# Performance work log

Measured on AMD Instinct MI355X. Metric: run time of the kernel, lower is better.

## Reference

```python
import jax, jax.numpy as jnp
import numpy as np

B, S, H = 2, 2048, 2048
NH, NKV, HD = 16, 8, 128        # head_dim = H // NH
WINDOW = 1024                    # sliding window size
THETA = 100000.0                 # rope_theta (RotaryEmbedding base)


def setup_inputs() -> dict:
    key = jax.random.key(0)
    ks = jax.random.split(key, 5)
    hidden = jax.random.normal(ks[0], (B, S, H), jnp.float32)
    # fused QKV projection: [H, NH*HD + 2*NKV*HD]
    W_pack = jax.random.normal(ks[1], (H, NH * HD + 2 * NKV * HD), jnp.float32) * (H ** -0.5)
    W_o = jax.random.normal(ks[2], (NH * HD, H), jnp.float32) * ((NH * HD) ** -0.5)
    # per-KV-head 2-tap causal conv weights, softmax-normalized (as in nn.Parameter init)
    conv_k = jax.nn.softmax(jax.random.normal(ks[3], (NKV, 2), jnp.float32), axis=-1)
    conv_v = jax.nn.softmax(jax.random.normal(ks[4], (NKV, 2), jnp.float32), axis=-1)
    return {"hidden": hidden, "W_pack": W_pack, "W_o": W_o, "conv_k": conv_k, "conv_v": conv_v}


def _rope(x, cos, sin):
    # x: (b, s, h, d); cos/sin: (s, d//2); non-interleaved (rotate-half) form
    d2 = x.shape[-1] // 2
    x1, x2 = x[..., :d2], x[..., d2:]
    c = cos[None, :, None, :]
    s = sin[None, :, None, :]
    return jnp.concatenate([x1 * c - x2 * s, x2 * c + x1 * s], axis=-1)


def _causal_conv2(x, w):
    # x: (b, s, kv, d); w: (kv, 2). out[t] = w0*x[t-1] + w1*x[t], zero-padded at t=0
    x_prev = jnp.pad(x, ((0, 0), (1, 0), (0, 0), (0, 0)))[:, :-1]
    return w[None, None, :, 0:1] * x_prev + w[None, None, :, 1:2] * x


def reference(hidden, W_pack, W_o, conv_k, conv_v):
    b, s, _ = hidden.shape
    qkv = hidden @ W_pack                                  # (b, s, NH*HD + 2*NKV*HD)
    q = qkv[..., : NH * HD].reshape(b, s, NH, HD)
    k = qkv[..., NH * HD : NH * HD + NKV * HD].reshape(b, s, NKV, HD)
    v = qkv[..., NH * HD + NKV * HD :].reshape(b, s, NKV, HD)

    inv_freq = 1.0 / (THETA ** (jnp.arange(0, HD, 2, dtype=jnp.float32) / HD))
    freqs = jnp.outer(jnp.arange(s, dtype=jnp.float32), inv_freq)  # (s, HD/2)
    cos, sin = jnp.cos(freqs), jnp.sin(freqs)
    q = _rope(q, cos, sin)
    k = _rope(k, cos, sin)

    # learned 2-tap causal conv mixing adjacent K/V states, per KV head
    k = _causal_conv2(k, conv_k)
    v = _causal_conv2(v, conv_v)

    # GQA: repeat kv heads to match query heads
    group = NH // NKV
    k = jnp.repeat(k, group, axis=2)  # (b, s, NH, HD)
    v = jnp.repeat(v, group, axis=2)

    scores = jnp.einsum('bqhd,bkhd->bhqk', q, k) / jnp.sqrt(jnp.float32(HD))
    i = jnp.arange(s)[:, None]
    j = jnp.arange(s)[None, :]
    mask = (j <= i) & (i - j < WINDOW)  # causal sliding-window mask
    scores = jnp.where(mask[None, None], scores, jnp.finfo(scores.dtype).min)
    probs = jax.nn.softmax(scores, axis=-1)
    out = jnp.einsum('bhqk,bkhd->bqhd', probs, v).reshape(b, s, NH * HD)
    return out @ W_o
```

## Files before the change

kernel.cpp:

```cpp
#include <hip/hip_runtime.h>

#define DI __device__ __forceinline__

typedef unsigned short u16;
typedef __attribute__((ext_vector_type(8))) short s16x8;
typedef __attribute__((ext_vector_type(8))) unsigned short u16x8;
typedef __attribute__((ext_vector_type(4))) float f32x4;
typedef __attribute__((ext_vector_type(16))) float f32x16;

DI u16 f2bf(float x) {
  union { float f; unsigned u; } a; a.f = x;
  unsigned r = a.u + 0x7FFFu + ((a.u >> 16) & 1u);
  return (u16)(r >> 16);
}
DI float bf2f(u16 u) {
  union { unsigned u; float f; } a; a.u = ((unsigned)u) << 16;
  return a.f;
}
DI void gload16(const void* g, void* l) {
  __builtin_amdgcn_global_load_lds(
      (const __attribute__((address_space(1))) unsigned int*)g,
      (__attribute__((address_space(3))) unsigned int*)l, 16, 0, 0);
}
DI f32x4 mfma16(s16x8 a, s16x8 b, f32x4 c) {
  return __builtin_amdgcn_mfma_f32_16x16x32_bf16(a, b, c, 0, 0, 0);
}
DI f32x16 mfma32(s16x8 a, s16x8 b, f32x16 c) {
  return __builtin_amdgcn_mfma_f32_32x32x16_bf16(a, b, c, 0, 0, 0);
}

DI void store4(u16* p, f32x4 v) {
  union { u16 u[4]; unsigned long long ll; } o;
  o.u[0] = f2bf(v[0]); o.u[1] = f2bf(v[1]); o.u[2] = f2bf(v[2]); o.u[3] = f2bf(v[3]);
  *(unsigned long long*)p = o.ll;
}
DI void store4(float* p, f32x4 v) { *(f32x4*)p = v; }

#define SBAR() asm volatile("s_barrier" ::: "memory")

__global__ __launch_bounds__(256) void prep_kernel(
    const float* __restrict__ hidden, const float* __restrict__ W_pack,
    const float* __restrict__ W_o, u16* __restrict__ hA, u16* __restrict__ wpT,
    u16* __restrict__ woT, float* __restrict__ cosT, float* __restrict__ sinT) {
  int bi = blockIdx.x;
  int t = threadIdx.x;
  if (bi < 4096) {
    int i = bi * 256 + t;
    const float4* p = (const float4*)hidden + (size_t)i * 2;
    float4 a = p[0], b = p[1];
    u16x8 o;
    o[0] = f2bf(a.x); o[1] = f2bf(a.y); o[2] = f2bf(a.z); o[3] = f2bf(a.w);
    o[4] = f2bf(b.x); o[5] = f2bf(b.y); o[6] = f2bf(b.z); o[7] = f2bf(b.w);
    *((u16x8*)hA + i) = o;
  } else if (bi < 7168) {
    const float* W; u16* Wt; int R, C, c0, r0;
    if (bi < 6144) {
      int idx = bi - 4096;
      W = W_pack; Wt = wpT; R = 2048; C = 4096;
      c0 = (idx & 63) * 64; r0 = (idx >> 6) * 64;
    } else {
      int idx = bi - 6144;
      W = W_o; Wt = woT; R = 2048; C = 2048;
      c0 = (idx & 31) * 64; r0 = (idx >> 5) * 64;
    }
    __shared__ u16 tile[64][65];
#pragma unroll
    for (int i = 0; i < 16; ++i) {
      int flat = i * 256 + t;
      int r = flat >> 6, c = flat & 63;
      tile[r][c] = f2bf(W[(size_t)(r0 + r) * C + (c0 + c)]);
    }
    __syncthreads();
#pragma unroll
    for (int i = 0; i < 16; ++i) {
      int flat = i * 256 + t;
      int c = flat >> 6, r = flat & 63;
      Wt[(size_t)(c0 + c) * R + (r0 + r)] = tile[r][c];
    }
  } else {
    int i = (bi - 7168) * 256 + t;
    int s = i >> 6, d = i & 63;
    float inv = expf(-(float)d * (11.5129254649702295f / 64.f));
    float f = (float)s * inv;
    cosT[i] = cosf(f);
    sinT[i] = sinf(f);
  }
}

template <typename OutT>
__global__ __launch_bounds__(512, 2) void gemm8p_kernel(
    const u16* __restrict__ A, const u16* __restrict__ Bt, OutT* __restrict__ C,
    int M, int N, int K) {
  __shared__ __align__(16) char lds[131072];
  int nwg = gridDim.x;
  int bid = blockIdx.x;
  int cpx = nwg >> 3;
  int swz = (bid & 7) * cpx + (bid >> 3);
  int ntn = N >> 8;
  int bm = swz / ntn, bn = swz - bm * ntn;
  int m0 = bm << 8, n0 = bn << 8;
  int t = threadIdx.x, w = t >> 6, l = t & 63;
  int wm = w >> 2, wn = w & 3;
  int NT = K >> 6;

  unsigned offA[2][2], offB[2][2];
  int cA[2][2], cB[2][2];
#pragma unroll
  for (int h = 0; h < 2; ++h)
#pragma unroll
    for (int i = 0; i < 2; ++i) {
      int c = i * 16 + h * 8 + w;
      cA[h][i] = c;
      int d = c * 1024 + l * 16;
      int s = d ^ ((((d >> 7) & 7)) << 4);
      offA[h][i] = (unsigned)(m0 + (s >> 7)) * (unsigned)(K * 2) + (unsigned)(s & 127);
      int c2 = ((w >> 2) << 3) + (w & 3) + h * 4 + i * 16;
      cB[h][i] = c2;
      int d2 = c2 * 1024 + l * 16;
      int s2 = d2 ^ ((((d2 >> 7) & 7)) << 4);
      offB[h][i] = (unsigned)(n0 + (s2 >> 7)) * (unsigned)(K * 2) + (unsigned)(s2 & 127);
    }
  const char* Ab = (const char*)A;
  const char* Bb = (const char*)Bt;

#define STAGE_A(tile, h) do { int _t = (tile); if (_t < NT) {                  \
    unsigned _k = (unsigned)_t * 128u;                                          \
    char* _ba = lds + ((_t & 1) << 16);                                         \
    gload16(Ab + (size_t)(offA[h][0] + _k), _ba + cA[h][0] * 1024);             \
    gload16(Ab + (size_t)(offA[h][1] + _k), _ba + cA[h][1] * 1024); } } while (0)
#define STAGE_B(tile, h) do { int _t = (tile); if (_t < NT) {                  \
    unsigned _k = (unsigned)_t * 128u;                                          \
    char* _bb = lds + ((_t & 1) << 16) + 32768;                                 \
    gload16(Bb + (size_t)(offB[h][0] + _k), _bb + cB[h][0] * 1024);             \
    gload16(Bb + (size_t)(offB[h][1] + _k), _bb + cB[h][1] * 1024); } } while (0)

  int hi = l >> 5;
  int rowb = (l & 31) << 7;
  unsigned lmix = (((unsigned)(l & 7) << 4) ^ ((unsigned)hi << 4));

  f32x16 acc[4][2] = {};
  s16x8 af[2][4], bf0[4], bf1[4];

  STAGE_A(0, 0); STAGE_B(0, 0); STAGE_A(0, 1); STAGE_B(0, 1);
  STAGE_A(1, 0); STAGE_B(1, 0); STAGE_A(1, 1);
  asm volatile("s_waitcnt vmcnt(6)" ::: "memory");
  SBAR();

  for (int tt = 0; tt < NT; ++tt) {
    const char* ldsA = lds + ((tt & 1) << 16);
    const char* ldsB = ldsA + 32768;
    const char* Ard = ldsA + (wm << 14) + rowb;
    const char* Brd = ldsB + (wn << 13) + rowb;

#pragma unroll
    for (int mb = 0; mb < 2; ++mb)
#pragma unroll
      for (int kc = 0; kc < 4; ++kc)
        af[mb][kc] = *(const s16x8*)(Ard + mb * 4096 + (lmix ^ (unsigned)(kc << 5)));
#pragma unroll
    for (int kc = 0; kc < 4; ++kc)
      bf0[kc] = *(const s16x8*)(Brd + (lmix ^ (unsigned)(kc << 5)));
    STAGE_B(tt + 1, 1);
    SBAR();
    __builtin_amdgcn_s_setprio(1);
#pragma unroll
    for (int kc = 0; kc < 4; ++kc) {
      acc[0][0] = mfma32(bf0[kc], af[0][kc], acc[0][0]);
      acc[1][0] = mfma32(bf0[kc], af[1][kc], acc[1][0]);
    }
    __builtin_amdgcn_s_setprio(0);
    SBAR();

#pragma unroll
    for (int kc = 0; kc < 4; ++kc)
      bf1[kc] = *(const s16x8*)(Brd + 4096 + (lmix ^ (unsigned)(kc << 5)));
    STAGE_A(tt + 2, 0);
    SBAR();
    __builtin_amdgcn_s_setprio(1);
#pragma unroll
    for (int kc = 0; kc < 4; ++kc) {
      acc[0][1] = mfma32(bf1[kc], af[0][kc], acc[0][1]);
      acc[1][1] = mfma32(bf1[kc], af[1][kc], acc[1][1]);
    }
    __builtin_amdgcn_s_setprio(0);
    SBAR();

#pragma unroll
    for (int mb = 0; mb < 2; ++mb)
#pragma unroll
      for (int kc = 0; kc < 4; ++kc)
        af[mb][kc] = *(const s16x8*)(Ard + 8192 + mb * 4096 + (lmix ^ (unsigned)(kc << 5)));
    STAGE_B(tt + 2, 0);
    SBAR();
    __builtin_amdgcn_s_setprio(1);
#pragma unroll
    for (int kc = 0; kc < 4; ++kc) {
      acc[2][0] = mfma32(bf0[kc], af[0][kc], acc[2][0]);
      acc[3][0] = mfma32(bf0[kc], af[1][kc], acc[3][0]);
    }
    __builtin_amdgcn_s_setprio(0);
    SBAR();

    STAGE_A(tt + 2, 1);
    SBAR();
    __builtin_amdgcn_s_setprio(1);
#pragma unroll
    for (int kc = 0; kc < 4; ++kc) {
      acc[2][1] = mfma32(bf1[kc], af[0][kc], acc[2][1]);
      acc[3][1] = mfma32(bf1[kc], af[1][kc], acc[3][1]);
    }
    __builtin_amdgcn_s_setprio(0);
    if (tt < NT - 2) asm volatile("s_waitcnt vmcnt(6)" ::: "memory");
    else             asm volatile("s_waitcnt vmcnt(0)" ::: "memory");
    SBAR();
  }
#undef STAGE_A
#undef STAGE_B

#pragma unroll
  for (int mb = 0; mb < 4; ++mb) {
    int row = m0 + wm * 128 + mb * 32 + (l & 31);
#pragma unroll
    for (int nb = 0; nb < 2; ++nb) {
      OutT* crow = C + (size_t)row * N + n0 + wn * 64 + nb * 32 + 4 * hi;
      f32x16 v = acc[mb][nb];
#pragma unroll
      for (int g = 0; g < 4; ++g) {
        f32x4 sv = { v[4 * g], v[4 * g + 1], v[4 * g + 2], v[4 * g + 3] };
        store4(crow + g * 8, sv);
      }
    }
  }
}

__global__ __launch_bounds__(512, 2) void gemm8pn_kernel(
    const u16* __restrict__ A, const u16* __restrict__ Bt, float* __restrict__ C,
    int M, int N, int K) {
  __shared__ __align__(16) char lds[98304];
  int nwg = gridDim.x;
  int bid = blockIdx.x;
  int cpx = nwg >> 3;
  int swz = (bid & 7) * cpx + (bid >> 3);
  int ntn = N >> 7;
  int bm = swz / ntn, bn = swz - bm * ntn;
  int m0 = bm << 8, n0 = bn << 7;
  int t = threadIdx.x, w = t >> 6, l = t & 63;
  int wm = w >> 2, wn = w & 3;
  int NT = K >> 6;

  unsigned offA[4], offB[2];
  int cA[4], cB[2];
#pragma unroll
  for (int u = 0; u < 4; ++u) {
    int c = u * 8 + w;
    cA[u] = c;
    int d = c * 1024 + l * 16;
    int s = d ^ ((((d >> 7) & 7)) << 4);
    offA[u] = (unsigned)(m0 + (s >> 7)) * (unsigned)(K * 2) + (unsigned)(s & 127);
  }
#pragma unroll
  for (int u = 0; u < 2; ++u) {
    int c = u * 8 + w;
    cB[u] = c;
    int d = c * 1024 + l * 16;
    int s = d ^ ((((d >> 7) & 7)) << 4);
    offB[u] = (unsigned)(n0 + (s >> 7)) * (unsigned)(K * 2) + (unsigned)(s & 127);
  }
  const char* Ab = (const char*)A;
  const char* Bb = (const char*)Bt;

#define STG_A(tile, u) do { int _t = (tile); if (_t < NT) {                    \
    gload16(Ab + (size_t)(offA[u] + (unsigned)_t * 128u),                       \
            lds + (_t & 1) * 49152 + cA[u] * 1024); } } while (0)
#define STG_B(tile, u) do { int _t = (tile); if (_t < NT) {                    \
    gload16(Bb + (size_t)(offB[u] + (unsigned)_t * 128u),                       \
            lds + (_t & 1) * 49152 + 32768 + cB[u] * 1024); } } while (0)

  int lanemix = ((l & 15) << 7) + ((((l >> 4) << 4) ^ ((l & 7) << 4)));
  int lanemix1 = lanemix ^ 64;

  f32x4 acc[8][2] = {};
  s16x8 af[4][2], bf0[2], bf1[2];

  STG_A(0, 0); STG_A(0, 1); STG_A(0, 2); STG_A(0, 3); STG_B(0, 0); STG_B(0, 1);
  STG_A(1, 0); STG_A(1, 1); STG_A(1, 2); STG_A(1, 3); STG_B(1, 0); STG_B(1, 1);
  asm volatile("s_waitcnt vmcnt(6)" ::: "memory");
  SBAR();

  for (int tt = 0; tt < NT; ++tt) {
    const char* ldsA = lds + (tt & 1) * 49152;
    const char* ldsB = ldsA + 32768;
    const char* Ard0 = ldsA + (wm << 14) + lanemix;
    const char* Ard1 = ldsA + (wm << 14) + lanemix1;
    const char* Brd0 = ldsB + (wn << 12) + lanemix;
    const char* Brd1 = ldsB + (wn << 12) + lanemix1;

#pragma unroll
    for (int mf = 0; mf < 4; ++mf) {
      af[mf][0] = *(const s16x8*)(Ard0 + mf * 2048);
      af[mf][1] = *(const s16x8*)(Ard1 + mf * 2048);
    }
    bf0[0] = *(const s16x8*)(Brd0);
    bf0[1] = *(const s16x8*)(Brd1);
    SBAR();
    __builtin_amdgcn_s_setprio(1);
#pragma unroll
    for (int mf = 0; mf < 4; ++mf) {
      acc[mf][0] = mfma16(bf0[0], af[mf][0], acc[mf][0]);
      acc[mf][0] = mfma16(bf0[1], af[mf][1], acc[mf][0]);
    }
    __builtin_amdgcn_s_setprio(0);
    SBAR();

    bf1[0] = *(const s16x8*)(Brd0 + 2048);
    bf1[1] = *(const s16x8*)(Brd1 + 2048);
    STG_A(tt + 2, 0); STG_A(tt + 2, 2);
    SBAR();
    __builtin_amdgcn_s_setprio(1);
#pragma unroll
    for (int mf = 0; mf < 4; ++mf) {
      acc[mf][1] = mfma16(bf1[0], af[mf][0], acc[mf][1]);
      acc[mf][1] = mfma16(bf1[1], af[mf][1], acc[mf][1]);
    }
    __builtin_amdgcn_s_setprio(0);
    SBAR();

#pragma unroll
    for (int mf = 0; mf < 4; ++mf) {
      af[mf][0] = *(const s16x8*)(Ard0 + (mf + 4) * 2048);
      af[mf][1] = *(const s16x8*)(Ard1 + (mf + 4) * 2048);
    }
    STG_B(tt + 2, 0); STG_B(tt + 2, 1);
    SBAR();
    __builtin_amdgcn_s_setprio(1);
#pragma unroll
    for (int mf = 0; mf < 4; ++mf) {
      acc[mf + 4][0] = mfma16(bf0[0], af[mf][0], acc[mf + 4][0]);
      acc[mf + 4][0] = mfma16(bf0[1], af[mf][1], acc[mf + 4][0]);
    }
    __builtin_amdgcn_s_setprio(0);
    SBAR();

    STG_A(tt + 2, 1); STG_A(tt + 2, 3);
    SBAR();
    __builtin_amdgcn_s_setprio(1);
#pragma unroll
    for (int mf = 0; mf < 4; ++mf) {
      acc[mf + 4][1] = mfma16(bf1[0], af[mf][0], acc[mf + 4][1]);
      acc[mf + 4][1] = mfma16(bf1[1], af[mf][1], acc[mf + 4][1]);
    }
    __builtin_amdgcn_s_setprio(0);
    if (tt < NT - 2) asm volatile("s_waitcnt vmcnt(6)" ::: "memory");
    else             asm volatile("s_waitcnt vmcnt(0)" ::: "memory");
    SBAR();
  }
#undef STG_A
#undef STG_B

#pragma unroll
  for (int mf = 0; mf < 8; ++mf) {
    int row = m0 + wm * 128 + mf * 16 + (l & 15);
    float* crow = C + (size_t)row * N + n0 + wn * 32 + (l >> 4) * 4;
#pragma unroll
    for (int nf = 0; nf < 2; ++nf) store4(crow + nf * 16, acc[mf][nf]);
  }
}

__global__ void rcvt_kernel(const u16* __restrict__ qkv, const float* __restrict__ cosT,
                            const float* __restrict__ sinT, const float* __restrict__ convk,
                            const float* __restrict__ convv,
                            u16* __restrict__ qb, u16* __restrict__ kb,
                            u16* __restrict__ vt) {
  int t = threadIdx.x;
  if (blockIdx.x < 4096) {
    const float qs = 0.08838834764831845f;
    int row = blockIdx.x;
    int b = row >> 11, s = row & 2047;
    const u16* qr = qkv + (size_t)row * 4096;
    u16* qo = qb + (size_t)row * 2048;
#pragma unroll
    for (int i = 0; i < 4; ++i) {
      int p = i * 256 + t;
      int h = p >> 6, d = p & 63;
      float x1 = bf2f(qr[h * 128 + d]), x2 = bf2f(qr[h * 128 + 64 + d]);
      float c = cosT[s * 64 + d], sn = sinT[s * 64 + d];
      qo[h * 128 + d] = f2bf((x1 * c - x2 * sn) * qs);
      qo[h * 128 + 64 + d] = f2bf((x2 * c + x1 * sn) * qs);
    }
    const u16* kr = qr + 2048;
#pragma unroll
    for (int i = 0; i < 2; ++i) {
      int p = i * 256 + t;
      int h = p >> 6, d = p & 63;
      float c = cosT[s * 64 + d], sn = sinT[s * 64 + d];
      float x1 = bf2f(kr[h * 128 + d]), x2 = bf2f(kr[h * 128 + 64 + d]);
      float r1 = x1 * c - x2 * sn, r2 = x2 * c + x1 * sn;
      float p1 = 0.f, p2 = 0.f;
      if (s > 0) {
        const u16* kp = kr - 4096;
        float cp = cosT[(s - 1) * 64 + d], sp = sinT[(s - 1) * 64 + d];
        float y1 = bf2f(kp[h * 128 + d]), y2 = bf2f(kp[h * 128 + 64 + d]);
        p1 = y1 * cp - y2 * sp;
        p2 = y2 * cp + y1 * sp;
      }
      float w0 = convk[h * 2], w1 = convk[h * 2 + 1];
      size_t o = (((size_t)b * 8 + h) * 2048 + s) * 128;
      kb[o + d] = f2bf(w0 * p1 + w1 * r1);
      kb[o + 64 + d] = f2bf(w0 * p2 + w1 * r2);
    }
  } else {
    __shared__ u16 lt[128][72];
    int idx = blockIdx.x - 4096;
    int st = idx & 31, bh = idx >> 5;
    int b = bh >> 3, h = bh & 7;
    int s0 = st * 64;
    float w0 = convv[h * 2], w1 = convv[h * 2 + 1];
#pragma unroll
    for (int i = 0; i < 32; ++i) {
      int flat = i * 256 + t;
      int sl = flat >> 7, d = flat & 127;
      int s = s0 + sl;
      int row = b * 2048 + s;
      float x = bf2f(qkv[(size_t)row * 4096 + 3072 + h * 128 + d]);
      float xp = (s > 0) ? bf2f(qkv[(size_t)(row - 1) * 4096 + 3072 + h * 128 + d]) : 0.f;
      lt[d][sl] = f2bf(w0 * xp + w1 * x);
    }
    __syncthreads();
#pragma unroll
    for (int i = 0; i < 32; ++i) {
      int flat = i * 256 + t;
      int d = flat >> 6, sl = flat & 63;
      vt[((size_t)(b * 8 + h) * 128 + d) * 2048 + s0 + sl] = lt[d][sl];
    }
  }
}

__global__ __launch_bounds__(256, 2) void attn2_kernel(
    const u16* __restrict__ qb, const u16* __restrict__ kbuf, const u16* __restrict__ vt,
    u16* __restrict__ ao) {
  __shared__ __align__(16) char lds[65536];
  int qt = blockIdx.x, bh = blockIdx.y;
  int b = bh >> 4, h = bh & 15, kh = h >> 1;
  int t = threadIdx.x, w = t >> 6, l = t & 63;
  int i0 = qt * 128;
  int qbase = i0 + w * 32;
  int lq = l & 31, hi = l >> 5;
  int xorc = (l & 7) << 4;
  const char* Kg = (const char*)(kbuf + (size_t)(b * 8 + kh) * 2048 * 128);
  const char* Vg = (const char*)(vt + (size_t)(b * 8 + kh) * 128 * 2048);

  s16x8 qf[8];
  {
    const u16* qp = qb + ((size_t)(b * 2048 + qbase + lq)) * 2048 + h * 128 + 8 * hi;
#pragma unroll
    for (int kc = 0; kc < 8; ++kc) qf[kc] = *(const s16x8*)(qp + kc * 16);
  }

  unsigned ksrc[4], vsrc[4], kdst[4], vdst[4];
#pragma unroll
  for (int i = 0; i < 4; ++i) {
    int c = w * 4 + i;
    int row = c * 4 + (l >> 4);
    int colb = (l & 15) * 16;
    ksrc[i] = (unsigned)(row * 256 + (colb ^ ((row & 7) << 4)));
    kdst[i] = (unsigned)(c * 1024);
    int d = c * 8 + (l >> 3);
    int cb2 = (l & 7) * 16;
    vsrc[i] = (unsigned)(d * 4096 + (cb2 ^ ((d & 7) << 4)));
    vdst[i] = (unsigned)(16384 + c * 1024);
  }

#define STAGEKV(tile, buf) do { int _j2 = (tile) << 6;                          \
    char* _lb = lds + ((buf) << 15);                                             \
    const char* _ks = Kg + (size_t)_j2 * 256;                                    \
    const char* _vs = Vg + (size_t)_j2 * 2;                                      \
    gload16(_ks + ksrc[0], _lb + kdst[0]); gload16(_vs + vsrc[0], _lb + vdst[0]);\
    gload16(_ks + ksrc[1], _lb + kdst[1]); gload16(_vs + vsrc[1], _lb + vdst[1]);\
    gload16(_ks + ksrc[2], _lb + kdst[2]); gload16(_vs + vsrc[2], _lb + vdst[2]);\
    gload16(_ks + ksrc[3], _lb + kdst[3]); gload16(_vs + vsrc[3], _lb + vdst[3]);\
  } while (0)

  int lo = i0 - 1023; if (lo < 0) lo = 0;
  int tk0 = lo >> 6, tk1 = (i0 + 127) >> 6;

  f32x16 acco[4] = {};
  float ls0 = 0.f, ls1 = 0.f, ls2 = 0.f, ls3 = 0.f;

  int cur = 0;
  STAGEKV(tk0, 0);
  asm volatile("s_waitcnt vmcnt(0)" ::: "memory");
  SBAR();

  for (int tk = tk0; tk <= tk1; ++tk) {
    int j0 = tk << 6;
    if (tk < tk1) STAGEKV(tk + 1, cur ^ 1);
    bool relevant = (j0 <= qbase + 31) && (j0 + 63 >= qbase - 1023);
    if (relevant) {
      const char* Kl = lds + (cur << 15);
      const char* Vl = Kl + 16384;
      const char* Krow = Kl + lq * 256;
      f32x16 ps0 = {}, ps1 = {};
      __builtin_amdgcn_s_setprio(1);
#pragma unroll
      for (int kc = 0; kc < 8; ++kc) {
        s16x8 kf = *(const s16x8*)(Krow + ((kc * 32 + hi * 16) ^ xorc));
        ps0 = mfma32(kf, qf[kc], ps0);
      }
#pragma unroll
      for (int kc = 0; kc < 8; ++kc) {
        s16x8 kf = *(const s16x8*)(Krow + 8192 + ((kc * 32 + hi * 16) ^ xorc));
        ps1 = mfma32(kf, qf[kc], ps1);
      }
      __builtin_amdgcn_s_setprio(0);
      bool domask = (j0 + 63 > qbase) || (qbase + 31 - j0 >= 1024);
      int di0 = qbase + lq - j0;
      float pe[32];
#pragma unroll
      for (int r = 0; r < 16; ++r) {
        float s0 = ps0[r], s1 = ps1[r];
        if (domask) {
          int crow = (r & 3) + 8 * (r >> 2) + 4 * hi;
          if ((unsigned)(di0 - crow) >= 1024u) s0 = -1e30f;
          if ((unsigned)(di0 - 32 - crow) >= 1024u) s1 = -1e30f;
        }
        float e0 = __expf(s0), e1 = __expf(s1);
        pe[r] = e0; pe[16 + r] = e1;
        if ((r & 3) == 0) { ls0 += e0 + e1; }
        else if ((r & 3) == 1) { ls1 += e0 + e1; }
        else if ((r & 3) == 2) { ls2 += e0 + e1; }
        else { ls3 += e0 + e1; }
      }
      unsigned pk[16];
#pragma unroll
      for (int p = 0; p < 16; ++p) {
        asm("v_cvt_pk_bf16_f32 %0, %1, %2" : "=v"(pk[p]) : "v"(pe[2 * p]), "v"(pe[2 * p + 1]));
      }
      s16x8 pa[4];
#pragma unroll
      for (int ks = 0; ks < 4; ++ks) {
        int base = (ks >> 1) * 8 + (ks & 1) * 4;
        unsigned keep0 = hi ? pk[base + 2] : pk[base + 0];
        unsigned keep1 = hi ? pk[base + 3] : pk[base + 1];
        unsigned send0 = hi ? pk[base + 0] : pk[base + 2];
        unsigned send1 = hi ? pk[base + 1] : pk[base + 3];
        unsigned recv0 = (unsigned)__shfl_xor((int)send0, 32);
        unsigned recv1 = (unsigned)__shfl_xor((int)send1, 32);
        union { unsigned u[4]; s16x8 v; } pu;
        pu.u[0] = hi ? recv0 : keep0;
        pu.u[1] = hi ? recv1 : keep1;
        pu.u[2] = hi ? keep0 : recv0;
        pu.u[3] = hi ? keep1 : recv1;
        pa[ks] = pu.v;
      }
      __builtin_amdgcn_s_setprio(1);
#pragma unroll
      for (int db = 0; db < 4; ++db) {
        const char* Vrow = Vl + db * 4096 + lq * 128;
#pragma unroll
        for (int ks = 0; ks < 4; ++ks) {
          s16x8 vf = *(const s16x8*)(Vrow + ((ks * 32 + hi * 16) ^ xorc));
          acco[db] = mfma32(pa[ks], vf, acco[db]);
        }
      }
      __builtin_amdgcn_s_setprio(0);
    }
    asm volatile("s_waitcnt vmcnt(0)" ::: "memory");
    SBAR();
    cur ^= 1;
  }
#undef STAGEKV

  float lrow = (ls0 + ls1) + (ls2 + ls3);
  float lt2 = lrow + __shfl_xor(lrow, 32);
  float rinv = 1.f / lt2;
#pragma unroll
  for (int r = 0; r < 16; ++r) {
    int qidx = (r & 3) + 8 * (r >> 2) + 4 * hi;
    float rv = __shfl(rinv, qidx);
    int i = qbase + qidx;
    u16* orow = ao + ((size_t)(b * 2048 + i)) * 2048 + h * 128 + lq;
#pragma unroll
    for (int db = 0; db < 4; ++db)
      orow[db * 32] = f2bf(acco[db][r] * rv);
  }
}

extern "C" void kernel_launch(void* const* d_in, const int* in_sizes, int n_in,
                              void* d_out, int out_size, void* d_ws, size_t ws_size,
                              hipStream_t stream) {
  (void)in_sizes; (void)n_in; (void)out_size; (void)ws_size;
  const float* hidden = (const float*)d_in[0];
  const float* W_pack = (const float*)d_in[1];
  const float* W_o    = (const float*)d_in[2];
  const float* conv_k = (const float*)d_in[3];
  const float* conv_v = (const float*)d_in[4];

  char* ws = (char*)d_ws;
  const size_t MB = 1u << 20;
  u16* hA    = (u16*)(ws + 0);
  u16* wpT   = (u16*)(ws + 16 * MB);
  u16* woT   = (u16*)(ws + 32 * MB);
  u16* qkv   = (u16*)(ws + 40 * MB);
  u16* qb    = (u16*)(ws + 72 * MB);
  u16* kbuf  = (u16*)(ws + 88 * MB);
  u16* vtb   = (u16*)(ws + 96 * MB);
  float* cosT = (float*)(ws + 104 * MB);
  float* sinT = (float*)(ws + 104 * MB + 524288);
  u16* attnb = qkv;

  prep_kernel<<<7680, 256, 0, stream>>>(hidden, W_pack, W_o, hA, wpT, woT, cosT, sinT);
  gemm8p_kernel<u16><<<256, 512, 0, stream>>>(hA, wpT, qkv, 4096, 4096, 2048);
  rcvt_kernel<<<4608, 256, 0, stream>>>(qkv, cosT, sinT, conv_k, conv_v, qb, kbuf, vtb);
  attn2_kernel<<<dim3(16, 32), 256, 0, stream>>>(qb, kbuf, vtb, attnb);
  gemm8pn_kernel<<<256, 512, 0, stream>>>(attnb, woT, (float*)d_out,
                                          4096, 2048, 2048);
}
```

Baseline: 196.1 us.

## Rewrite QKV GEMM as 4-stage ring-buffered pipeline with 16x16 MFMA tiles

Replaces the double-buffered QKV projection GEMM, which used K-tiles of 64 and many intra-iteration barriers, with a four-slot LDS ring of K-tiles of 32 prefetched three tiles ahead. Each iteration now issues one barrier. The MFMA shape changes from 32x32 to 16x16 with an 8x4 fragment grid and a new swizzled LDS layout. The intent is to cut barrier count and deepen load/compute overlap. In exchange there are more LDS fragment reads per FLOP and smaller MFMA instructions, which could lower MFMA efficiency.

```diff
diff --git a/kernel.cpp b/kernel.cpp
--- a/kernel.cpp
+++ b/kernel.cpp
@@ -87,13 +87,12 @@
   }
 }
 
-template <typename OutT>
-__global__ __launch_bounds__(512, 2) void gemm8p_kernel(
-    const u16* __restrict__ A, const u16* __restrict__ Bt, OutT* __restrict__ C,
+__global__ __launch_bounds__(512, 2) void gemm_ring_kernel(
+    const u16* __restrict__ A, const u16* __restrict__ Bt, u16* __restrict__ C,
     int M, int N, int K) {
-  __shared__ __align__(16) char lds[131072];
-  int nwg = gridDim.x;
-  int bid = blockIdx.x;
+  constexpr int BSZ = 32768;
+  __shared__ __align__(16) char lds[4 * BSZ];
+  int nwg = gridDim.x, bid = blockIdx.x;
   int cpx = nwg >> 3;
   int swz = (bid & 7) * cpx + (bid >> 3);
   int ntn = N >> 8;
@@ -101,135 +100,68 @@
   int m0 = bm << 8, n0 = bn << 8;
   int t = threadIdx.x, w = t >> 6, l = t & 63;
   int wm = w >> 2, wn = w & 3;
-  int NT = K >> 6;
-
-  unsigned offA[2][2], offB[2][2];
-  int cA[2][2], cB[2][2];
-#pragma unroll
-  for (int h = 0; h < 2; ++h)
-#pragma unroll
-    for (int i = 0; i < 2; ++i) {
-      int c = i * 16 + h * 8 + w;
-      cA[h][i] = c;
-      int d = c * 1024 + l * 16;
-      int s = d ^ ((((d >> 7) & 7)) << 4);
-      offA[h][i] = (unsigned)(m0 + (s >> 7)) * (unsigned)(K * 2) + (unsigned)(s & 127);
-      int c2 = ((w >> 2) << 3) + (w & 3) + h * 4 + i * 16;
-      cB[h][i] = c2;
-      int d2 = c2 * 1024 + l * 16;
-      int s2 = d2 ^ ((((d2 >> 7) & 7)) << 4);
-      offB[h][i] = (unsigned)(n0 + (s2 >> 7)) * (unsigned)(K * 2) + (unsigned)(s2 & 127);
-    }
+  int NT = K >> 5;
+
+  unsigned srcA[2], srcB[2];
+  unsigned scol = (unsigned)(((t & 3) ^ ((t >> 3) & 3)) << 4);
+#pragma unroll
+  for (int u = 0; u < 2; ++u) {
+    srcA[u] = (unsigned)(m0 + u * 128 + (t >> 2)) * (unsigned)(K * 2) + scol;
+    srcB[u] = (unsigned)(n0 + u * 128 + (t >> 2)) * (unsigned)(K * 2) + scol;
+  }
+  unsigned dstT = (unsigned)(t * 16);
   const char* Ab = (const char*)A;
   const char* Bb = (const char*)Bt;
 
-#define STAGE_A(tile, h) do { int _t = (tile); if (_t < NT) {                  \
-    unsigned _k = (unsigned)_t * 128u;                                          \
-    char* _ba = lds + ((_t & 1) << 16);                                         \
-    gload16(Ab + (size_t)(offA[h][0] + _k), _ba + cA[h][0] * 1024);             \
-    gload16(Ab + (size_t)(offA[h][1] + _k), _ba + cA[h][1] * 1024); } } while (0)
-#define STAGE_B(tile, h) do { int _t = (tile); if (_t < NT) {                  \
-    unsigned _k = (unsigned)_t * 128u;                                          \
-    char* _bb = lds + ((_t & 1) << 16) + 32768;                                 \
-    gload16(Bb + (size_t)(offB[h][0] + _k), _bb + cB[h][0] * 1024);             \
-    gload16(Bb + (size_t)(offB[h][1] + _k), _bb + cB[h][1] * 1024); } } while (0)
-
-  int hi = l >> 5;
-  int rowb = (l & 31) << 7;
-  unsigned lmix = (((unsigned)(l & 7) << 4) ^ ((unsigned)hi << 4));
-
-  f32x16 acc[4][2] = {};
-  s16x8 af[2][4], bf0[4], bf1[4];
-
-  STAGE_A(0, 0); STAGE_B(0, 0); STAGE_A(0, 1); STAGE_B(0, 1);
-  STAGE_A(1, 0); STAGE_B(1, 0); STAGE_A(1, 1);
-  asm volatile("s_waitcnt vmcnt(6)" ::: "memory");
+#define STAGE(tile) do { int _t = (tile); if (_t < NT) {                        \
+    char* _bb = lds + (size_t)(_t & 3) * BSZ;                                    \
+    unsigned _k = (unsigned)_t * 64u;                                            \
+    gload16(Ab + (size_t)(srcA[0] + _k), _bb + dstT);                            \
+    gload16(Ab + (size_t)(srcA[1] + _k), _bb + 8192 + dstT);                     \
+    gload16(Bb + (size_t)(srcB[0] + _k), _bb + 16384 + dstT);                    \
+    gload16(Bb + (size_t)(srcB[1] + _k), _bb + 24576 + dstT);                    \
+  } } while (0)
+
+  int lanemix = ((l & 15) << 6) + ((((l >> 4) ^ ((l >> 1) & 3))) << 4);
+
+  f32x4 acc[8][4] = {};
+  s16x8 af[8], bfr[4];
+
+  STAGE(0); STAGE(1); STAGE(2);
+  asm volatile("s_waitcnt vmcnt(8)" ::: "memory");
   SBAR();
 
   for (int tt = 0; tt < NT; ++tt) {
-    const char* ldsA = lds + ((tt & 1) << 16);
-    const char* ldsB = ldsA + 32768;
-    const char* Ard = ldsA + (wm << 14) + rowb;
-    const char* Brd = ldsB + (wn << 13) + rowb;
-
-#pragma unroll
-    for (int mb = 0; mb < 2; ++mb)
-#pragma unroll
-      for (int kc = 0; kc < 4; ++kc)
-        af[mb][kc] = *(const s16x8*)(Ard + mb * 4096 + (lmix ^ (unsigned)(kc << 5)));
-#pragma unroll
-    for (int kc = 0; kc < 4; ++kc)
-      bf0[kc] = *(const s16x8*)(Brd + (lmix ^ (unsigned)(kc << 5)));
-    STAGE_B(tt + 1, 1);
-    SBAR();
+    char* buf = lds + (size_t)(tt & 3) * BSZ;
+    const char* Ard = buf + wm * 8192 + lanemix;
+    const char* Brd = buf + 16384 + wn * 4096 + lanemix;
+    STAGE(tt + 3);
+#pragma unroll
+    for (int mf = 0; mf < 8; ++mf) af[mf] = *(const s16x8*)(Ard + mf * 1024);
+#pragma unroll
+    for (int nf = 0; nf < 4; ++nf) bfr[nf] = *(const s16x8*)(Brd + nf * 1024);
     __builtin_amdgcn_s_setprio(1);
 #pragma unroll
-    for (int kc = 0; kc < 4; ++kc) {
-      acc[0][0] = mfma32(bf0[kc], af[0][kc], acc[0][0]);
-      acc[1][0] = mfma32(bf0[kc], af[1][kc], acc[1][0]);
-    }
+    for (int mf = 0; mf < 8; ++mf)
+#pragma unroll
+      for (int nf = 0; nf < 4; ++nf)
+        acc[mf][nf] = mfma16(bfr[nf], af[mf], acc[mf][nf]);
     __builtin_amdgcn_s_setprio(0);
-    SBAR();
-
-#pragma unroll
-    for (int kc = 0; kc < 4; ++kc)
-      bf1[kc] = *(const s16x8*)(Brd + 4096 + (lmix ^ (unsigned)(kc << 5)));
-    STAGE_A(tt + 2, 0);
-    SBAR();
-    __builtin_amdgcn_s_setprio(1);
-#pragma unroll
-    for (int kc = 0; kc < 4; ++kc) {
-      acc[0][1] = mfma32(bf1[kc], af[0][kc], acc[0][1]);
-      acc[1][1] = mfma32(bf1[kc], af[1][kc], acc[1][1]);
-    }
-    __builtin_amdgcn_s_setprio(0);
-    SBAR();
-
-#pragma unroll
-    for (int mb = 0; mb < 2; ++mb)
-#pragma unroll
-      for (int kc = 0; kc < 4; ++kc)
-        af[mb][kc] = *(const s16x8*)(Ard + 8192 + mb * 4096 + (lmix ^ (unsigned)(kc << 5)));
-    STAGE_B(tt + 2, 0);
-    SBAR();
-    __builtin_amdgcn_s_setprio(1);
-#pragma unroll
-    for (int kc = 0; kc < 4; ++kc) {
-      acc[2][0] = mfma32(bf0[kc], af[0][kc], acc[2][0]);
-      acc[3][0] = mfma32(bf0[kc], af[1][kc], acc[3][0]);
-    }
-    __builtin_amdgcn_s_setprio(0);
-    SBAR();
-
-    STAGE_A(tt + 2, 1);
-    SBAR();
-    __builtin_amdgcn_s_setprio(1);
-#pragma unroll
-    for (int kc = 0; kc < 4; ++kc) {
-      acc[2][1] = mfma32(bf1[kc], af[0][kc], acc[2][1]);
-      acc[3][1] = mfma32(bf1[kc], af[1][kc], acc[3][1]);
-    }
-    __builtin_amdgcn_s_setprio(0);
-    if (tt < NT - 2) asm volatile("s_waitcnt vmcnt(6)" ::: "memory");
-    else             asm volatile("s_waitcnt vmcnt(0)" ::: "memory");
-    SBAR();
-  }
-#undef STAGE_A
-#undef STAGE_B
-
-#pragma unroll
-  for (int mb = 0; mb < 4; ++mb) {
-    int row = m0 + wm * 128 + mb * 32 + (l & 31);
-#pragma unroll
-    for (int nb = 0; nb < 2; ++nb) {
-      OutT* crow = C + (size_t)row * N + n0 + wn * 64 + nb * 32 + 4 * hi;
-      f32x16 v = acc[mb][nb];
-#pragma unroll
-      for (int g = 0; g < 4; ++g) {
-        f32x4 sv = { v[4 * g], v[4 * g + 1], v[4 * g + 2], v[4 * g + 3] };
-        store4(crow + g * 8, sv);
-      }
-    }
+    if (tt + 1 < NT) {
+      if (tt + 3 < NT)      asm volatile("s_waitcnt vmcnt(8)" ::: "memory");
+      else if (tt + 2 < NT) asm volatile("s_waitcnt vmcnt(4)" ::: "memory");
+      else                  asm volatile("s_waitcnt vmcnt(0)" ::: "memory");
+      SBAR();
+    }
+  }
+#undef STAGE
+
+#pragma unroll
+  for (int mf = 0; mf < 8; ++mf) {
+    int row = m0 + wm * 128 + mf * 16 + (l & 15);
+    u16* crow = C + (size_t)row * N + n0 + wn * 64 + (l >> 4) * 4;
+#pragma unroll
+    for (int nf = 0; nf < 4; ++nf) store4(crow + nf * 16, acc[mf][nf]);
   }
 }
 
@@ -609,7 +541,7 @@
   u16* attnb = qkv;
 
   prep_kernel<<<7680, 256, 0, stream>>>(hidden, W_pack, W_o, hA, wpT, woT, cosT, sinT);
-  gemm8p_kernel<u16><<<256, 512, 0, stream>>>(hA, wpT, qkv, 4096, 4096, 2048);
+  gemm_ring_kernel<<<256, 512, 0, stream>>>(hA, wpT, qkv, 4096, 4096, 2048);
   rcvt_kernel<<<4608, 256, 0, stream>>>(qkv, cosT, sinT, conv_k, conv_v, qb, kbuf, vtb);
   attn2_kernel<<<dim3(16, 32), 256, 0, stream>>>(qb, kbuf, vtb, attnb);
   gemm8pn_kernel<<<256, 512, 0, stream>>>(attnb, woT, (float*)d_out,
```

New measurement: 191.0 us. 2.6% less time.
